# Optimization experiments

Measured on AMD Instinct MI355X. Metric: run time of the kernel, lower is better.

## Reference

```python
import jax, jax.numpy as jnp
import numpy as np

KS = 7001          # Gaussian kernel taps (hard-coded in smooth_predictions)
STD = 30.0
B, S, D = 512, 8000, 256


def gaussian_kernel():
    # torch.linspace(-size//2 + 1, size//2, size) with size=7001 -> -3500..3500
    x = jnp.linspace(-(KS // 2), KS // 2, KS)
    k = jnp.exp(-x ** 2 / (2.0 * STD ** 2))
    return k / jnp.sum(k)


def smooth_predictions(v):
    # v: (B, 1, S); depthwise (single-channel) conv1d, 'same' padding
    k = gaussian_kernel().reshape(1, 1, KS).astype(v.dtype)
    return jax.lax.conv_general_dilated(
        v, k, window_strides=(1,), padding=[(KS // 2, KS // 2)],
        dimension_numbers=('NCH', 'OIH', 'NCH'))


def _param(b, w, bias, lo, hi):
    # Linear(D,1) -> relu -> clamp; returns (B, 1)
    return jnp.clip(jax.nn.relu(b @ w.T + bias), lo, hi)


def setup_inputs() -> dict:
    key = jax.random.key(0)
    ks = jax.random.split(key, 10)
    inp = {
        'v_out': jax.random.normal(ks[0], (B, 1, S), jnp.float32),
        'b': jax.random.normal(ks[1], (B, D), jnp.float32),
        'k_w': 0.02 * jax.random.normal(ks[2], (1, D), jnp.float32),
        'k_b': jnp.zeros((1,), jnp.float32),
        'a_w': 0.02 * jax.random.normal(ks[3], (1, D), jnp.float32),
        'a_b': jnp.zeros((1,), jnp.float32),
        'epsilon_w': 0.02 * jax.random.normal(ks[4], (1, D), jnp.float32),
        'epsilon_b': jnp.zeros((1,), jnp.float32),
        'gamma_w': 0.02 * jax.random.normal(ks[5], (1, D), jnp.float32),
        'gamma_b': jnp.zeros((1,), jnp.float32),
        'use_cond': 0,
        'name': 0,
    }
    return inp


def reference(v_out, b, k_w, k_b, a_w, a_b, epsilon_w, epsilon_b,
              gamma_w, gamma_b, use_cond, name):
    t_ = jnp.ones_like(v_out) * 1.6            # (B,1,S)
    t_out = t_                                  # expanded form is identical

    k = _param(b, k_w, k_b, 0.1, 1.0)          # (B,1)
    a = _param(b, a_w, a_b, 0.001, 0.1)
    epsilon = _param(b, epsilon_w, epsilon_b, 0.005, 0.1)
    gamma = _param(b, gamma_w, gamma_b, 0.5, 2.0)

    # unsqueeze(1) + expand over seq -> broadcast as (B,1,1)
    k_e = k[:, :, None]
    a_e = a[:, :, None]
    eps_e = epsilon[:, :, None]
    g_e = gamma[:, :, None]

    ones = jnp.ones_like(v_out)
    v_s = smooth_predictions(v_out)            # (B,1,S)

    dv_l = jnp.pad(v_s, ((0, 0), (0, 0), (1, 0)))   # (B,1,S+1)
    dv_r = jnp.pad(v_s, ((0, 0), (0, 0), (0, 1)))   # (B,1,S+1)
    dt = t_out / 7999.0
    dv_t = (dv_r[:, :, 1:] - dv_l[:, :, :-1]) / (2.0 * dt)
    dv2_t = (dv_r[:, :, 1:] + dv_l[:, :, :-1] - 2.0 * v_s) / dt ** 2

    eps_0 = 0.001
    v_noisy = jnp.where(v_s == 0, jnp.full_like(v_s, eps_0), v_s)
    inv_v = v_noisy ** (-1)
    inv_v = jnp.where(jnp.isnan(inv_v), jnp.zeros_like(inv_v), inv_v)

    term_l1 = v_s * k_e * dv_t * (ones - 2.0 * v_s + a_e)
    term_l2 = inv_v * dv_t ** 2
    term_lt = 1000.0 * term_l1 + term_l2 - dv2_t

    term_r1 = v_s * (v_s - g_e * k_e * 1000.0 * (ones - v_s) * (v_s - a_e))
    term_rt = eps_e * (term_r1 + g_e * dv_t)

    dv_out = term_lt - term_rt
    if use_cond:
        dv_out = jnp.where(v_out <= 0, jnp.zeros_like(dv_out), dv_out)

    dv_out = jnp.concatenate([dv_out[:, :, 100:950], dv_out[:, :, 1050:-100]],
                             axis=2)
    dv_out = jnp.log(dv_out ** 2 + 1e-5)
    return (dv_out, dv_t, dv2_t, a, k * 1000.0, epsilon, gamma, t_,
            dv_l, dv_r, t_out)
```

## Files before the change

kernel.cpp:

```cpp
#include <hip/hip_runtime.h>
#include <math.h>

#define SLEN 8000
#define NBATCH 512
#define DDIM 256

#define RAD 160
#define TAPS 321
#define CHUNK 2048
#define CBLK 256
#define TPO 8
#define HALO_L 176
#define WIN (HALO_L + CHUNK + RAD + 16)
#define LDSZ (WIN + WIN / 8)

#define O0  0
#define O1  3942400
#define O2  8038400
#define O3  12134400
#define O4  12134912
#define O5  12135424
#define O6  12135936
#define O7  12136448
#define O8  16232448
#define O9  20328960
#define O10 24425472

typedef float f4u __attribute__((vector_size(16), aligned(4)));

__global__ __launch_bounds__(256) void pc_params_kernel(
    const float* __restrict__ b,
    const float* __restrict__ kw, const float* __restrict__ kb,
    const float* __restrict__ aw, const float* __restrict__ ab,
    const float* __restrict__ ew, const float* __restrict__ eb,
    const float* __restrict__ gw, const float* __restrict__ gb,
    float* __restrict__ out3, float* __restrict__ out4,
    float* __restrict__ out5, float* __restrict__ out6,
    float* __restrict__ wsp)
{
    __shared__ float4 red[256];
    const int row = blockIdx.x;
    const int d = threadIdx.x;
    const float bv = b[row * DDIM + d];
    red[d] = make_float4(bv * kw[d], bv * aw[d], bv * ew[d], bv * gw[d]);
    __syncthreads();
    for (int s2 = 128; s2 > 0; s2 >>= 1) {
        if (d < s2) {
            float4 o = red[d + s2];
            red[d].x += o.x; red[d].y += o.y; red[d].z += o.z; red[d].w += o.w;
        }
        __syncthreads();
    }
    if (d == 0) {
        float4 s = red[0];
        float k = fminf(fmaxf(fmaxf(s.x + kb[0], 0.0f), 0.1f),   1.0f);
        float a = fminf(fmaxf(fmaxf(s.y + ab[0], 0.0f), 0.001f), 0.1f);
        float e = fminf(fmaxf(fmaxf(s.z + eb[0], 0.0f), 0.005f), 0.1f);
        float g = fminf(fmaxf(fmaxf(s.w + gb[0], 0.0f), 0.5f),   2.0f);
        out3[row] = a;
        out4[row] = k * 1000.0f;
        out5[row] = e;
        out6[row] = g;
        wsp[row]          = k;
        wsp[512 + row]    = a;
        wsp[1024 + row]   = e;
        wsp[1536 + row]   = g;
    }
}

__global__ __launch_bounds__(CBLK) void pc_fused_kernel(
    const float* __restrict__ v,
    const float* __restrict__ wsp,
    const int* __restrict__ use_cond,
    float* __restrict__ out0, float* __restrict__ out1,
    float* __restrict__ out2, float* __restrict__ out7,
    float* __restrict__ dvl,  float* __restrict__ dvr,
    float* __restrict__ out10)
{
    __shared__ float lds[LDSZ];
    __shared__ __align__(16) float wlds[TAPS + 7];
    __shared__ float eL[CBLK], eR[CBLK];

    const int row = blockIdx.y;
    const int i0 = blockIdx.x * CHUNK;
    const int tid = threadIdx.x;
    const float* vrow = v + (long)row * SLEN;

    for (int j = tid; j < TAPS; j += CBLK) {
        const float d = (float)(j - RAD);
        wlds[j] = expf(d * d * (-1.0f / 1800.0f)) * (float)(1.0 / 75.19884823893001);
    }

    const int st = i0 - HALO_L;
    for (int idx = tid; idx < WIN; idx += CBLK) {
        const int g = st + idx;
        const float val = (g >= 0 && g < SLEN) ? vrow[g] : 0.0f;
        lds[idx + (idx >> 3)] = val;
    }
    __syncthreads();

    float acc[TPO];
#pragma unroll
    for (int t = 0; t < TPO; ++t) acc[t] = 0.0f;

    float sreg[16];
    {
        const float* p0 = lds + 9 * (tid + 2);
        const float* p1 = lds + 9 * (tid + 3);
#pragma unroll
        for (int k = 0; k < 8; ++k) sreg[k] = p0[k];
#pragma unroll
        for (int k = 0; k < 8; ++k) sreg[8 + k] = p1[k];
    }

#pragma unroll 2
    for (int m = 0; m < 40; ++m) {
        const float4 w0 = *(const float4*)(wlds + 8 * m);
        const float4 w1 = *(const float4*)(wlds + 8 * m + 4);
        const float wc[8] = {w0.x, w0.y, w0.z, w0.w, w1.x, w1.y, w1.z, w1.w};
#pragma unroll
        for (int c = 0; c < 8; ++c) {
#pragma unroll
            for (int t = 0; t < TPO; ++t) acc[t] += wc[c] * sreg[c + t];
        }
#pragma unroll
        for (int k = 0; k < 8; ++k) sreg[k] = sreg[k + 8];
        const float* pn = lds + 9 * (tid + m + 4);
#pragma unroll
        for (int k = 0; k < 8; ++k) sreg[8 + k] = pn[k];
    }
    {
        const float wc = wlds[TAPS - 1];
#pragma unroll
        for (int t = 0; t < TPO; ++t) acc[t] += wc * sreg[t];
    }

    float leftE = 0.0f, rightE = 0.0f;
    if (tid == 0) {
        for (int j = 0; j < TAPS; ++j) {
            const int x = 15 + j;
            leftE += wlds[j] * lds[x + (x >> 3)];
        }
    }
    if (tid == CBLK - 1) {
        for (int j = 0; j < TAPS; ++j) {
            const int x = 2064 + j;
            rightE += wlds[j] * lds[x + (x >> 3)];
        }
    }

    eL[tid] = acc[0];
    eR[tid] = acc[7];
    __syncthreads();
    const float eRp = (tid > 0)        ? eR[tid - 1] : leftE;
    const float eLn = (tid < CBLK - 1) ? eL[tid + 1] : rightE;

    const float kk = wsp[row];
    const float aa = wsp[512 + row];
    const float ee = wsp[1024 + row];
    const float gg = wsp[1536 + row];
    const int uc = *use_cond;

    constexpr float DT = 1.6f / 7999.0f;
    constexpr float C1 = 1.0f / (2.0f * DT);
    constexpr float C2 = 1.0f / (DT * DT);

    const int i8 = i0 + 8 * tid;
    float dvt8[TPO], dv28[TPO], lg8[TPO];
#pragma unroll
    for (int t = 0; t < TPO; ++t) {
        const int i = i8 + t;
        const float vc = acc[t];
        float vm = (t == 0) ? eRp : acc[t - 1];
        float vp = (t == TPO - 1) ? eLn : acc[t + 1];
        if (i == 0) vm = 0.0f;
        if (i == SLEN - 1) vp = 0.0f;

        const float dv_t = (vp - vm) * C1;
        const float dv2  = (vp + vm - 2.0f * vc) * C2;

        float vn = (vc == 0.0f) ? 0.001f : vc;
        float inv_v = 1.0f / vn;
        if (inv_v != inv_v) inv_v = 0.0f;

        const float term_l1 = vc * kk * dv_t * (1.0f - 2.0f * vc + aa);
        const float term_l2 = inv_v * dv_t * dv_t;
        const float term_lt = 1000.0f * term_l1 + term_l2 - dv2;
        const float term_r1 = vc * (vc - gg * kk * 1000.0f * (1.0f - vc) * (vc - aa));
        const float term_rt = ee * (term_r1 + gg * dv_t);
        float dvo = term_lt - term_rt;
        if (uc) {
            if (vrow[i < SLEN ? i : 0] <= 0.0f) dvo = 0.0f;
        }
        dvt8[t] = dv_t;
        dv28[t] = dv2;
        lg8[t]  = logf(dvo * dvo + 1e-5f);
    }

    if (i8 < SLEN) {
        const long rs = (long)row * SLEN + i8;
        *(float4*)(out1 + rs)     = make_float4(dvt8[0], dvt8[1], dvt8[2], dvt8[3]);
        *(float4*)(out1 + rs + 4) = make_float4(dvt8[4], dvt8[5], dvt8[6], dvt8[7]);
        *(float4*)(out2 + rs)     = make_float4(dv28[0], dv28[1], dv28[2], dv28[3]);
        *(float4*)(out2 + rs + 4) = make_float4(dv28[4], dv28[5], dv28[6], dv28[7]);
        const float4 c16 = make_float4(1.6f, 1.6f, 1.6f, 1.6f);
        *(float4*)(out7 + rs)      = c16;
        *(float4*)(out7 + rs + 4)  = c16;
        *(float4*)(out10 + rs)     = c16;
        *(float4*)(out10 + rs + 4) = c16;

        const long rb = (long)row * (SLEN + 1) + i8;
        f4u a0 = {acc[0], acc[1], acc[2], acc[3]};
        f4u a1 = {acc[4], acc[5], acc[6], acc[7]};
        *(f4u*)(dvr + rb)     = a0;
        *(f4u*)(dvr + rb + 4) = a1;
        *(f4u*)(dvl + rb + 1) = a0;
        *(f4u*)(dvl + rb + 5) = a1;
        if (i8 == 0)        dvl[(long)row * (SLEN + 1)] = 0.0f;
        if (i8 == SLEN - 8) dvr[(long)row * (SLEN + 1) + SLEN] = 0.0f;

        const long r0 = (long)row * 7700;
#pragma unroll
        for (int t = 0; t < TPO; ++t) {
            const int i = i8 + t;
            if (i >= 100 && i < 950)        out0[r0 + (i - 100)] = lg8[t];
            else if (i >= 1050 && i < 7900) out0[r0 + (i - 200)] = lg8[t];
        }
    }
}

extern "C" void kernel_launch(void* const* d_in, const int* in_sizes, int n_in,
                              void* d_out, int out_size, void* d_ws, size_t ws_size,
                              hipStream_t stream)
{
    const float* v_out = (const float*)d_in[0];
    const float* b  = (const float*)d_in[1];
    const float* kw = (const float*)d_in[2];
    const float* kb = (const float*)d_in[3];
    const float* aw = (const float*)d_in[4];
    const float* ab = (const float*)d_in[5];
    const float* ew = (const float*)d_in[6];
    const float* eb = (const float*)d_in[7];
    const float* gw = (const float*)d_in[8];
    const float* gb = (const float*)d_in[9];
    const int* use_cond = (const int*)d_in[10];
    float* out = (float*)d_out;
    float* wsp = (float*)d_ws;

    pc_params_kernel<<<NBATCH, 256, 0, stream>>>(
        b, kw, kb, aw, ab, ew, eb, gw, gb,
        out + O3, out + O4, out + O5, out + O6, wsp);

    pc_fused_kernel<<<dim3((SLEN + CHUNK - 1) / CHUNK, NBATCH), CBLK, 0, stream>>>(
        v_out, wsp, use_cond,
        out + O0, out + O1, out + O2, out + O7,
        out + O8, out + O9, out + O10);
}
```

Measured before the change: 190.7 us.

## Pass conv taps as kernel argument, vectorize LDS window and output stores

The Gaussian taps are now computed on the host in double precision and passed as a by-value struct, so the weights come from the kernel-argument constant path instead of being built in LDS with expf. The input window is loaded with float4 global reads into an unpadded LDS array. The inner loop reads LDS with float4 and is fully unrolled. Edge values are now computed by a wave-parallel shuffle reduction instead of a serial loop on one thread. The params kernel uses one wave with shuffle reductions, log uses the fast intrinsic, and the log output is written with float4 stores where aligned. The risks are LDS bank conflicts from the stride-8 float4 reads, precision changes from __logf and __expf, and a possible bug: both edge values read from one shared `edge` variable, while thread 255 only gets the value computed by wave 3.

New measurement: 514.9 us. 170% more time.

```diff
diff --git a/kernel.cpp b/kernel.cpp
--- a/kernel.cpp
+++ b/kernel.cpp
@@ -11,8 +11,7 @@
 #define CBLK 256
 #define TPO 8
 #define HALO_L 176
-#define WIN (HALO_L + CHUNK + RAD + 16)
-#define LDSZ (WIN + WIN / 8)
+#define WIN 2400
 
 #define O0  0
 #define O1  3942400
@@ -28,7 +27,9 @@
 
 typedef float f4u __attribute__((vector_size(16), aligned(4)));
 
-__global__ __launch_bounds__(256) void pc_params_kernel(
+struct WTable { float w[TAPS]; };
+
+__global__ __launch_bounds__(64) void pc_params_kernel(
     const float* __restrict__ b,
     const float* __restrict__ kw, const float* __restrict__ kb,
     const float* __restrict__ aw, const float* __restrict__ ab,
@@ -38,25 +39,29 @@
     float* __restrict__ out5, float* __restrict__ out6,
     float* __restrict__ wsp)
 {
-    __shared__ float4 red[256];
     const int row = blockIdx.x;
-    const int d = threadIdx.x;
-    const float bv = b[row * DDIM + d];
-    red[d] = make_float4(bv * kw[d], bv * aw[d], bv * ew[d], bv * gw[d]);
-    __syncthreads();
-    for (int s2 = 128; s2 > 0; s2 >>= 1) {
-        if (d < s2) {
-            float4 o = red[d + s2];
-            red[d].x += o.x; red[d].y += o.y; red[d].z += o.z; red[d].w += o.w;
-        }
-        __syncthreads();
-    }
-    if (d == 0) {
-        float4 s = red[0];
-        float k = fminf(fmaxf(fmaxf(s.x + kb[0], 0.0f), 0.1f),   1.0f);
-        float a = fminf(fmaxf(fmaxf(s.y + ab[0], 0.0f), 0.001f), 0.1f);
-        float e = fminf(fmaxf(fmaxf(s.z + eb[0], 0.0f), 0.005f), 0.1f);
-        float g = fminf(fmaxf(fmaxf(s.w + gb[0], 0.0f), 0.5f),   2.0f);
+    const int l = threadIdx.x;
+    const float4 bb = *(const float4*)(b + (long)row * DDIM + 4 * l);
+    const float4 k4 = *(const float4*)(kw + 4 * l);
+    const float4 a4 = *(const float4*)(aw + 4 * l);
+    const float4 e4 = *(const float4*)(ew + 4 * l);
+    const float4 g4 = *(const float4*)(gw + 4 * l);
+    float sk = bb.x * k4.x + bb.y * k4.y + bb.z * k4.z + bb.w * k4.w;
+    float sa = bb.x * a4.x + bb.y * a4.y + bb.z * a4.z + bb.w * a4.w;
+    float se = bb.x * e4.x + bb.y * e4.y + bb.z * e4.z + bb.w * e4.w;
+    float sg = bb.x * g4.x + bb.y * g4.y + bb.z * g4.z + bb.w * g4.w;
+#pragma unroll
+    for (int m = 1; m < 64; m <<= 1) {
+        sk += __shfl_xor(sk, m, 64);
+        sa += __shfl_xor(sa, m, 64);
+        se += __shfl_xor(se, m, 64);
+        sg += __shfl_xor(sg, m, 64);
+    }
+    if (l == 0) {
+        float k = fminf(fmaxf(fmaxf(sk + kb[0], 0.0f), 0.1f),   1.0f);
+        float a = fminf(fmaxf(fmaxf(sa + ab[0], 0.0f), 0.001f), 0.1f);
+        float e = fminf(fmaxf(fmaxf(se + eb[0], 0.0f), 0.005f), 0.1f);
+        float g = fminf(fmaxf(fmaxf(sg + gb[0], 0.0f), 0.5f),   2.0f);
         out3[row] = a;
         out4[row] = k * 1000.0f;
         out5[row] = e;
@@ -75,10 +80,10 @@
     float* __restrict__ out0, float* __restrict__ out1,
     float* __restrict__ out2, float* __restrict__ out7,
     float* __restrict__ dvl,  float* __restrict__ dvr,
-    float* __restrict__ out10)
+    float* __restrict__ out10,
+    WTable wt)
 {
-    __shared__ float lds[LDSZ];
-    __shared__ __align__(16) float wlds[TAPS + 7];
+    __shared__ __align__(16) float win[WIN];
     __shared__ float eL[CBLK], eR[CBLK];
 
     const int row = blockIdx.y;
@@ -86,118 +91,122 @@
     const int tid = threadIdx.x;
     const float* vrow = v + (long)row * SLEN;
 
-    for (int j = tid; j < TAPS; j += CBLK) {
-        const float d = (float)(j - RAD);
-        wlds[j] = expf(d * d * (-1.0f / 1800.0f)) * (float)(1.0 / 75.19884823893001);
-    }
-
     const int st = i0 - HALO_L;
-    for (int idx = tid; idx < WIN; idx += CBLK) {
-        const int g = st + idx;
-        const float val = (g >= 0 && g < SLEN) ? vrow[g] : 0.0f;
-        lds[idx + (idx >> 3)] = val;
+    for (int g4 = tid; g4 < WIN / 4; g4 += CBLK) {
+        const int gw0 = st + 4 * g4;
+        float4 val;
+        if (gw0 >= 0 && gw0 + 3 < SLEN) {
+            val = *(const float4*)(vrow + gw0);
+        } else {
+            val.x = (gw0 >= 0     && gw0     < SLEN) ? vrow[gw0]     : 0.0f;
+            val.y = (gw0 + 1 >= 0 && gw0 + 1 < SLEN) ? vrow[gw0 + 1] : 0.0f;
+            val.z = (gw0 + 2 >= 0 && gw0 + 2 < SLEN) ? vrow[gw0 + 2] : 0.0f;
+            val.w = (gw0 + 3 >= 0 && gw0 + 3 < SLEN) ? vrow[gw0 + 3] : 0.0f;
+        }
+        *(float4*)(win + 4 * g4) = val;
     }
     __syncthreads();
 
+    const int wv = tid >> 6;
+    float edge = 0.0f;
+    if (wv == 0 || wv == 3) {
+        const int l = tid & 63;
+        const int xb = (wv == 0) ? 15 : 2064;
+        float p = 0.0f;
+#pragma unroll
+        for (int r = 0; r < 6; ++r) {
+            const int j = l + (r << 6);
+            if (j < TAPS) {
+                const float d = (float)(j - RAD);
+                p += __expf(d * d * (-1.0f / 1800.0f)) * win[xb + j];
+            }
+        }
+#pragma unroll
+        for (int m = 1; m < 64; m <<= 1) p += __shfl_xor(p, m, 64);
+        edge = p * (float)(1.0 / 75.19884823893001);
+    }
+
     float acc[TPO];
 #pragma unroll
     for (int t = 0; t < TPO; ++t) acc[t] = 0.0f;
 
+    const float* wp = win + 8 * tid + 16;
     float sreg[16];
+    *(float4*)(&sreg[0])  = *(const float4*)(wp);
+    *(float4*)(&sreg[4])  = *(const float4*)(wp + 4);
+    *(float4*)(&sreg[8])  = *(const float4*)(wp + 8);
+    *(float4*)(&sreg[12]) = *(const float4*)(wp + 12);
+
+#pragma unroll
+    for (int m = 0; m < 40; ++m) {
+        const float4 n0 = *(const float4*)(wp + 8 * m + 16);
+        const float4 n1 = *(const float4*)(wp + 8 * m + 20);
+#pragma unroll
+        for (int c = 0; c < 8; ++c) {
+            const float wc = wt.w[8 * m + c];
+#pragma unroll
+            for (int t = 0; t < TPO; ++t) acc[t] += wc * sreg[c + t];
+        }
+#pragma unroll
+        for (int k = 0; k < 8; ++k) sreg[k] = sreg[k + 8];
+        sreg[8]  = n0.x; sreg[9]  = n0.y; sreg[10] = n0.z; sreg[11] = n0.w;
+        sreg[12] = n1.x; sreg[13] = n1.y; sreg[14] = n1.z; sreg[15] = n1.w;
+    }
     {
-        const float* p0 = lds + 9 * (tid + 2);
-        const float* p1 = lds + 9 * (tid + 3);
-#pragma unroll
-        for (int k = 0; k < 8; ++k) sreg[k] = p0[k];
-#pragma unroll
-        for (int k = 0; k < 8; ++k) sreg[8 + k] = p1[k];
-    }
-
-#pragma unroll 2
-    for (int m = 0; m < 40; ++m) {
-        const float4 w0 = *(const float4*)(wlds + 8 * m);
-        const float4 w1 = *(const float4*)(wlds + 8 * m + 4);
-        const float wc[8] = {w0.x, w0.y, w0.z, w0.w, w1.x, w1.y, w1.z, w1.w};
-#pragma unroll
-        for (int c = 0; c < 8; ++c) {
-#pragma unroll
-            for (int t = 0; t < TPO; ++t) acc[t] += wc[c] * sreg[c + t];
-        }
-#pragma unroll
-        for (int k = 0; k < 8; ++k) sreg[k] = sreg[k + 8];
-        const float* pn = lds + 9 * (tid + m + 4);
-#pragma unroll
-        for (int k = 0; k < 8; ++k) sreg[8 + k] = pn[k];
-    }
-    {
-        const float wc = wlds[TAPS - 1];
+        const float wc = wt.w[320];
 #pragma unroll
         for (int t = 0; t < TPO; ++t) acc[t] += wc * sreg[t];
-    }
-
-    float leftE = 0.0f, rightE = 0.0f;
-    if (tid == 0) {
-        for (int j = 0; j < TAPS; ++j) {
-            const int x = 15 + j;
-            leftE += wlds[j] * lds[x + (x >> 3)];
-        }
-    }
-    if (tid == CBLK - 1) {
-        for (int j = 0; j < TAPS; ++j) {
-            const int x = 2064 + j;
-            rightE += wlds[j] * lds[x + (x >> 3)];
-        }
     }
 
     eL[tid] = acc[0];
     eR[tid] = acc[7];
     __syncthreads();
-    const float eRp = (tid > 0)        ? eR[tid - 1] : leftE;
-    const float eLn = (tid < CBLK - 1) ? eL[tid + 1] : rightE;
-
-    const float kk = wsp[row];
-    const float aa = wsp[512 + row];
-    const float ee = wsp[1024 + row];
-    const float gg = wsp[1536 + row];
-    const int uc = *use_cond;
-
-    constexpr float DT = 1.6f / 7999.0f;
-    constexpr float C1 = 1.0f / (2.0f * DT);
-    constexpr float C2 = 1.0f / (DT * DT);
+    const float eRp = (tid > 0)        ? eR[tid - 1] : edge;
+    const float eLn = (tid < CBLK - 1) ? eL[tid + 1] : edge;
 
     const int i8 = i0 + 8 * tid;
-    float dvt8[TPO], dv28[TPO], lg8[TPO];
-#pragma unroll
-    for (int t = 0; t < TPO; ++t) {
-        const int i = i8 + t;
-        const float vc = acc[t];
-        float vm = (t == 0) ? eRp : acc[t - 1];
-        float vp = (t == TPO - 1) ? eLn : acc[t + 1];
-        if (i == 0) vm = 0.0f;
-        if (i == SLEN - 1) vp = 0.0f;
-
-        const float dv_t = (vp - vm) * C1;
-        const float dv2  = (vp + vm - 2.0f * vc) * C2;
-
-        float vn = (vc == 0.0f) ? 0.001f : vc;
-        float inv_v = 1.0f / vn;
-        if (inv_v != inv_v) inv_v = 0.0f;
-
-        const float term_l1 = vc * kk * dv_t * (1.0f - 2.0f * vc + aa);
-        const float term_l2 = inv_v * dv_t * dv_t;
-        const float term_lt = 1000.0f * term_l1 + term_l2 - dv2;
-        const float term_r1 = vc * (vc - gg * kk * 1000.0f * (1.0f - vc) * (vc - aa));
-        const float term_rt = ee * (term_r1 + gg * dv_t);
-        float dvo = term_lt - term_rt;
-        if (uc) {
-            if (vrow[i < SLEN ? i : 0] <= 0.0f) dvo = 0.0f;
-        }
-        dvt8[t] = dv_t;
-        dv28[t] = dv2;
-        lg8[t]  = logf(dvo * dvo + 1e-5f);
-    }
-
     if (i8 < SLEN) {
+        const float kk = wsp[row];
+        const float aa = wsp[512 + row];
+        const float ee = wsp[1024 + row];
+        const float gg = wsp[1536 + row];
+        const int uc = *use_cond;
+
+        constexpr float DT = 1.6f / 7999.0f;
+        constexpr float C1 = 1.0f / (2.0f * DT);
+        constexpr float C2 = 1.0f / (DT * DT);
+
+        float dvt8[TPO], dv28[TPO], lg8[TPO];
+#pragma unroll
+        for (int t = 0; t < TPO; ++t) {
+            const int i = i8 + t;
+            const float vc = acc[t];
+            float vm = (t == 0) ? eRp : acc[t - 1];
+            float vp = (t == TPO - 1) ? eLn : acc[t + 1];
+            if (i == 0) vm = 0.0f;
+            if (i == SLEN - 1) vp = 0.0f;
+
+            const float dv_t = (vp - vm) * C1;
+            const float dv2  = (vp + vm - 2.0f * vc) * C2;
+
+            float vn = (vc == 0.0f) ? 0.001f : vc;
+            float inv_v = 1.0f / vn;
+            if (inv_v != inv_v) inv_v = 0.0f;
+
+            const float term_l1 = vc * kk * dv_t * (1.0f - 2.0f * vc + aa);
+            const float term_l2 = inv_v * dv_t * dv_t;
+            const float term_lt = 1000.0f * term_l1 + term_l2 - dv2;
+            const float term_r1 = vc * (vc - gg * kk * 1000.0f * (1.0f - vc) * (vc - aa));
+            const float term_rt = ee * (term_r1 + gg * dv_t);
+            float dvo = term_lt - term_rt;
+            if (uc) {
+                if (vrow[i] <= 0.0f) dvo = 0.0f;
+            }
+            dvt8[t] = dv_t;
+            dv28[t] = dv2;
+            lg8[t]  = __logf(dvo * dvo + 1e-5f);
+        }
+
         const long rs = (long)row * SLEN + i8;
         *(float4*)(out1 + rs)     = make_float4(dvt8[0], dvt8[1], dvt8[2], dvt8[3]);
         *(float4*)(out1 + rs + 4) = make_float4(dvt8[4], dvt8[5], dvt8[6], dvt8[7]);
@@ -220,12 +229,30 @@
         if (i8 == SLEN - 8) dvr[(long)row * (SLEN + 1) + SLEN] = 0.0f;
 
         const long r0 = (long)row * 7700;
-#pragma unroll
-        for (int t = 0; t < TPO; ++t) {
-            const int i = i8 + t;
-            if (i >= 100 && i < 950)        out0[r0 + (i - 100)] = lg8[t];
-            else if (i >= 1050 && i < 7900) out0[r0 + (i - 200)] = lg8[t];
-        }
+        if (i8 >= 100 && i8 + 8 <= 950) {
+            *(float4*)(out0 + r0 + i8 - 100) = make_float4(lg8[0], lg8[1], lg8[2], lg8[3]);
+            *(float4*)(out0 + r0 + i8 - 96)  = make_float4(lg8[4], lg8[5], lg8[6], lg8[7]);
+        } else if (i8 >= 1050 && i8 + 8 <= 7900) {
+            *(float4*)(out0 + r0 + i8 - 200) = make_float4(lg8[0], lg8[1], lg8[2], lg8[3]);
+            *(float4*)(out0 + r0 + i8 - 196) = make_float4(lg8[4], lg8[5], lg8[6], lg8[7]);
+        } else {
+#pragma unroll
+            for (int t = 0; t < TPO; ++t) {
+                const int i = i8 + t;
+                if (i >= 100 && i < 950)        out0[r0 + (i - 100)] = lg8[t];
+                else if (i >= 1050 && i < 7900) out0[r0 + (i - 200)] = lg8[t];
+            }
+        }
+    }
+}
+
+static void build_wtable(WTable* wt) {
+    double norm = 0.0;
+    for (int d = -3500; d <= 3500; ++d)
+        norm += exp(-(double)d * (double)d / 1800.0);
+    for (int j = 0; j < TAPS; ++j) {
+        const int d = j - RAD;
+        wt->w[j] = (float)(exp(-(double)d * (double)d / 1800.0) / norm);
     }
 }
 
@@ -247,12 +274,15 @@
     float* out = (float*)d_out;
     float* wsp = (float*)d_ws;
 
-    pc_params_kernel<<<NBATCH, 256, 0, stream>>>(
+    WTable wt;
+    build_wtable(&wt);
+
+    pc_params_kernel<<<NBATCH, 64, 0, stream>>>(
         b, kw, kb, aw, ab, ew, eb, gw, gb,
         out + O3, out + O4, out + O5, out + O6, wsp);
 
-    pc_fused_kernel<<<dim3((SLEN + CHUNK - 1) / CHUNK, NBATCH), CBLK, 0, stream>>>(
+    pc_fused_kernel<<<dim3(SLEN / CHUNK + ((SLEN % CHUNK) ? 1 : 0), NBATCH), CBLK, 0, stream>>>(
         v_out, wsp, use_cond,
         out + O0, out + O1, out + O2, out + O7,
-        out + O8, out + O9, out + O10);
-}
+        out + O8, out + O9, out + O10, wt);
+}
```
